# Performance work log

Measured on AMD Instinct MI355X. Metric: run time of the kernel, lower is better.

## Reference

```python
import jax, jax.numpy as jnp
import numpy as np
from jax import lax

EPS = 1e-5

def conv2d(x, w):
    # x: [B,C,H,W], w: [O,I,kh,kw], VALID, stride 1
    return lax.conv_general_dilated(x, w, (1, 1), 'VALID',
                                    dimension_numbers=('NCHW', 'OIHW', 'NCHW'))

def bn_eval(x, g, b, m, v):
    # per-channel eval-mode batchnorm on NCHW
    scale = g / jnp.sqrt(v + EPS)
    return x * scale[None, :, None, None] + (b - m * scale)[None, :, None, None]

def xcorr_depthwise(search, kernel):
    # search: [B,C,Hs,Ws], kernel: [B,C,hk,wk] -> [B,C,Ho,Wo]
    B, C, Hs, Ws = search.shape
    hk, wk = kernel.shape[2], kernel.shape[3]
    s = search.reshape(1, B * C, Hs, Ws)
    k = kernel.reshape(B * C, 1, hk, wk)
    out = lax.conv_general_dilated(s, k, (1, 1), 'VALID',
                                   dimension_numbers=('NCHW', 'OIHW', 'NCHW'),
                                   feature_group_count=B * C)
    return out.reshape(B, C, out.shape[2], out.shape[3])

def setup_inputs() -> dict:
    key = jax.random.key(0)
    ks = jax.random.split(key, 16)
    B, C, HID, OUT = 64, 256, 256, 10
    d = {}
    d['kernel'] = jax.random.normal(ks[0], (B, C, 7, 7), jnp.float32)
    d['search'] = jax.random.normal(ks[1], (B, C, 31, 31), jnp.float32)
    # conv_kernel branch
    d['ck_w'] = jax.random.normal(ks[2], (HID, C, 3, 3), jnp.float32) * 0.02
    d['ck_g'] = jnp.ones((HID,), jnp.float32)
    d['ck_b'] = jnp.zeros((HID,), jnp.float32)
    d['ck_m'] = jax.random.normal(ks[3], (HID,), jnp.float32) * 0.1
    d['ck_v'] = jax.random.uniform(ks[4], (HID,), jnp.float32, 0.5, 1.5)
    # conv_search branch
    d['cs_w'] = jax.random.normal(ks[5], (HID, C, 3, 3), jnp.float32) * 0.02
    d['cs_g'] = jnp.ones((HID,), jnp.float32)
    d['cs_b'] = jnp.zeros((HID,), jnp.float32)
    d['cs_m'] = jax.random.normal(ks[6], (HID,), jnp.float32) * 0.1
    d['cs_v'] = jax.random.uniform(ks[7], (HID,), jnp.float32, 0.5, 1.5)
    # head: 1x1 conv (no bias) + BN + ReLU + 1x1 conv (bias)
    d['h1_w'] = jax.random.normal(ks[8], (HID, HID), jnp.float32) * 0.05
    d['h_g'] = jnp.ones((HID,), jnp.float32)
    d['h_b'] = jnp.zeros((HID,), jnp.float32)
    d['h_m'] = jax.random.normal(ks[9], (HID,), jnp.float32) * 0.1
    d['h_v'] = jax.random.uniform(ks[10], (HID,), jnp.float32, 0.5, 1.5)
    d['h2_w'] = jax.random.normal(ks[11], (OUT, HID), jnp.float32) * 0.05
    d['h2_b'] = jnp.zeros((OUT,), jnp.float32)
    return d

def reference(kernel, search, ck_w, ck_g, ck_b, ck_m, ck_v,
              cs_w, cs_g, cs_b, cs_m, cs_v,
              h1_w, h_g, h_b, h_m, h_v, h2_w, h2_b):
    k = jax.nn.relu(bn_eval(conv2d(kernel, ck_w), ck_g, ck_b, ck_m, ck_v))   # [B,256,5,5]
    s = jax.nn.relu(bn_eval(conv2d(search, cs_w), cs_g, cs_b, cs_m, cs_v))   # [B,256,29,29]
    feat = xcorr_depthwise(s, k)                                             # [B,256,25,25]
    x = jnp.einsum('oi,bihw->bohw', h1_w, feat)
    x = jax.nn.relu(bn_eval(x, h_g, h_b, h_m, h_v))
    out = jnp.einsum('oi,bihw->bohw', h2_w, x) + h2_b[None, :, None, None]   # [B,10,25,25]
    return out
```

## Files before the change

kernel.cpp:

```cpp
#include <hip/hip_runtime.h>
#include <cstddef>
#include <cstdint>

#define BN_EPS 1e-5f

typedef __attribute__((ext_vector_type(8))) __bf16 bf16x8;
typedef __attribute__((ext_vector_type(4))) float f32x4;

__device__ inline unsigned short f2bf(float f) {
    unsigned u = __builtin_bit_cast(unsigned, f);
    unsigned r = (u + 0x7fff + ((u >> 16) & 1)) >> 16;
    return (unsigned short)r;
}
__device__ inline float bf2f(unsigned short u) {
    return __builtin_bit_cast(float, (unsigned)u << 16);
}

#define GLDS16(g, l)                                                        \
    __builtin_amdgcn_global_load_lds(                                       \
        (const __attribute__((address_space(1))) void*)(g),                 \
        (__attribute__((address_space(3))) void*)(l), 16, 0, 0)

template<int H, int W, int WP>
__device__ inline void nhwc_body(int bh, const float* __restrict__ in,
                                 unsigned short* __restrict__ out)
{
    __shared__ unsigned short tl[256][WP];
    const int tid = threadIdx.x;
    const int b = bh / H, h = bh - b * H;
    const int g = tid >> 5, wl = tid & 31;
    const float* base = in + (size_t)b * 256 * (H * W) + (size_t)h * W;
    if (wl < W) {
        #pragma unroll
        for (int cc = 0; cc < 32; ++cc) {
            const int c = cc * 8 + g;
            tl[c][wl] = f2bf(base[(size_t)c * (H * W) + wl]);
        }
    }
    __syncthreads();
    unsigned short* dst = out + (size_t)bh * W * 256 + tid;
    #pragma unroll
    for (int w = 0; w < W; ++w) dst[w * 256] = tl[tid][w];
}

__global__ __launch_bounds__(256)
void prep_kernel(const float* __restrict__ srch, const float* __restrict__ kin,
                 const float* __restrict__ cs_w, const float* __restrict__ ck_w,
                 const float* __restrict__ h1_w, const float* __restrict__ h2_w,
                 unsigned short* __restrict__ s16, unsigned short* __restrict__ k16,
                 unsigned short* __restrict__ wTs, unsigned short* __restrict__ wTk,
                 unsigned short* __restrict__ h1w16, unsigned short* __restrict__ h2w16,
                 int G31, int G7)
{
    const int bid = blockIdx.x;
    if (bid < G31) {
        nhwc_body<31, 31, 33>(bid, srch, s16);
    } else if (bid < G31 + G7) {
        nhwc_body<7, 7, 9>(bid - G31, kin, k16);
    } else {
        const int i = (bid - G31 - G7) * 256 + threadIdx.x;
        if (i < 589824) {
            const int ic = i & 255, t = i >> 8, oc = t & 255, khkw = t >> 8;
            wTs[i] = f2bf(cs_w[(size_t)((oc << 8) + ic) * 9 + khkw]);
        } else if (i < 1179648) {
            const int j = i - 589824;
            const int ic = j & 255, t = j >> 8, oc = t & 255, khkw = t >> 8;
            wTk[j] = f2bf(ck_w[(size_t)((oc << 8) + ic) * 9 + khkw]);
        } else if (i < 1245184) {
            const int j = i - 1179648;
            h1w16[j] = f2bf(h1_w[j]);
        } else if (i < 1249280) {
            const int j = i - 1245184;
            const int oc = j >> 8, ic = j & 255;
            h2w16[j] = (oc < 10) ? f2bf(h2_w[oc * 256 + ic]) : (unsigned short)0;
        }
    }
}

struct ConvParams {
    const unsigned short* bsrc;
    const unsigned short* wT;
    const float *bg, *bb, *bm, *bv;
    unsigned short* out;
    int IH, IW, OW, PPB, N;
};

__global__ __launch_bounds__(256)
void conv3x3_kernel(ConvParams S, ConvParams K, int Gs)
{
    __shared__ __align__(16) unsigned short Alds[128 * 64];
    __shared__ __align__(16) unsigned short Blds[128 * 64];

    const int tid  = threadIdx.x;
    const int lane = tid & 63;
    const int wid  = tid >> 6;

    const int raw = blockIdx.x;
    ConvParams P;
    int tileid;
    if (raw < Gs) {
        P = S;
        const int q8 = Gs >> 3, r8 = Gs & 7;
        const int xcd = raw & 7, seq = raw >> 3;
        tileid = (xcd < r8 ? xcd * (q8 + 1) : r8 * (q8 + 1) + (xcd - r8) * q8) + seq;
    } else {
        P = K;
        tileid = raw - Gs;
    }
    const int pt  = tileid >> 1;
    const int oct = tileid & 1;
    const int oc0 = oct << 7;
    const int p0  = pt << 7;

    int aoff[4], brow[4], bgs8[4], ldsrow[4];
    #pragma unroll
    for (int i = 0; i < 4; ++i) {
        const int r  = i * 32 + wid * 8 + (lane >> 3);
        const int gs = (lane & 7) ^ (r & 7);
        aoff[i] = (oc0 + r) * 256 + gs * 8;
        int pg = p0 + r; if (pg > P.N - 1) pg = P.N - 1;
        const int bb_ = pg / P.PPB;
        const int p   = pg - bb_ * P.PPB;
        const int oh  = p / P.OW, ow = p - oh * P.OW;
        brow[i] = (bb_ * P.IH + oh) * P.IW + ow;
        bgs8[i] = gs * 8;
        ldsrow[i] = (i * 32 + wid * 8) * 64;
    }

    const int q_  = lane >> 4;
    const int lr  = lane & 15;
    const int wm0 = (wid >> 1) * 64;
    const int wn0 = (wid & 1) * 64;
    const int g0  = q_ ^ (lane & 7);
    const int g1  = (4 + q_) ^ (lane & 7);
    const unsigned short* Abase = &Alds[(wm0 + lr) * 64];
    const unsigned short* Bbase = &Blds[(wn0 + lr) * 64];

    f32x4 acc[4][4] = {};

    int kh = 0, kw = 0;
    for (int khkw = 0; khkw < 9; ++khkw) {
        const size_t wslice = (size_t)khkw << 16;
        const int tapadd = kh * P.IW + kw;
        for (int ics = 0; ics < 4; ++ics) {
            const int ic0 = ics * 64;
            __syncthreads();
            #pragma unroll
            for (int i = 0; i < 4; ++i) {
                GLDS16(P.wT + wslice + aoff[i] + ic0, &Alds[ldsrow[i]]);
                GLDS16(P.bsrc + (size_t)(brow[i] + tapadd) * 256 + ic0 + bgs8[i],
                       &Blds[ldsrow[i]]);
            }
            __syncthreads();

            bf16x8 bfr[4][2];
            #pragma unroll
            for (int n = 0; n < 4; ++n) {
                bfr[n][0] = *(const bf16x8*)(Bbase + n * 1024 + g0 * 8);
                bfr[n][1] = *(const bf16x8*)(Bbase + n * 1024 + g1 * 8);
            }
            #pragma unroll
            for (int m = 0; m < 4; ++m) {
                bf16x8 a0 = *(const bf16x8*)(Abase + m * 1024 + g0 * 8);
                bf16x8 a1 = *(const bf16x8*)(Abase + m * 1024 + g1 * 8);
                #pragma unroll
                for (int n = 0; n < 4; ++n) {
                    acc[m][n] = __builtin_amdgcn_mfma_f32_16x16x32_bf16(
                                    a0, bfr[n][0], acc[m][n], 0, 0, 0);
                    acc[m][n] = __builtin_amdgcn_mfma_f32_16x16x32_bf16(
                                    a1, bfr[n][1], acc[m][n], 0, 0, 0);
                }
            }
        }
        if (++kw == 3) { kw = 0; ++kh; }
    }

    #pragma unroll
    for (int m = 0; m < 4; ++m) {
        const int ocm = oc0 + wm0 + m * 16 + q_ * 4;
        float sc[4], sh[4];
        #pragma unroll
        for (int r = 0; r < 4; ++r) {
            sc[r] = P.bg[ocm + r] * rsqrtf(P.bv[ocm + r] + BN_EPS);
            sh[r] = P.bb[ocm + r] - P.bm[ocm + r] * sc[r];
        }
        #pragma unroll
        for (int n = 0; n < 4; ++n) {
            const int pg = p0 + wn0 + n * 16 + lr;
            if (pg < P.N) {
                unsigned e0 = f2bf(fmaxf(acc[m][n][0] * sc[0] + sh[0], 0.f));
                unsigned e1 = f2bf(fmaxf(acc[m][n][1] * sc[1] + sh[1], 0.f));
                unsigned e2 = f2bf(fmaxf(acc[m][n][2] * sc[2] + sh[2], 0.f));
                unsigned e3 = f2bf(fmaxf(acc[m][n][3] * sc[3] + sh[3], 0.f));
                uint2 v; v.x = e0 | (e1 << 16); v.y = e2 | (e3 << 16);
                *(uint2*)(P.out + (size_t)pg * 256 + ocm) = v;
            }
        }
    }
}

__global__ __launch_bounds__(256)
void xcorr_nhwc_kernel(const unsigned short* __restrict__ sfeat,
                       const unsigned short* __restrict__ kfeat,
                       unsigned short* __restrict__ xc2)
{
    const int bid = blockIdx.x;
    const int b = bid / 25, oh = bid - b * 25;
    const int c = threadIdx.x;

    float kv[25];
    const unsigned short* kp = kfeat + (size_t)b * 25 * 256 + c;
    #pragma unroll
    for (int t = 0; t < 25; ++t) kv[t] = bf2f(kp[t * 256]);

    float acc[25];
    #pragma unroll
    for (int ow = 0; ow < 25; ++ow) acc[ow] = 0.f;

    const unsigned short* sp = sfeat + ((size_t)(b * 29 + oh)) * 29 * 256 + c;
    #pragma unroll
    for (int i = 0; i < 5; ++i) {
        #pragma unroll
        for (int w = 0; w < 29; ++w) {
            const float sv = bf2f(sp[(i * 29 + w) * 256]);
            #pragma unroll
            for (int j = 0; j < 5; ++j) {
                if (j <= w && w - j <= 24)
                    acc[w - j] += sv * kv[i * 5 + j];
            }
        }
    }

    unsigned short* op = xc2 + ((size_t)(b * 625 + oh * 25)) * 256 + c;
    #pragma unroll
    for (int ow = 0; ow < 25; ++ow) op[ow * 256] = f2bf(acc[ow]);
}

template<int KH, int KW, int IH, int IW, int OW, int PPB, bool OUT_NT>
__global__ __launch_bounds__(256)
void conv_mfma_kernel(const unsigned short* __restrict__ bsrc,
                      const unsigned short* __restrict__ wT,
                      const float* __restrict__ bn_g,
                      const float* __restrict__ bn_b,
                      const float* __restrict__ bn_m,
                      const float* __restrict__ bn_v,
                      float* __restrict__ out_f32,
                      unsigned short* __restrict__ out_nt,
                      int N)
{
    constexpr int KHW = KH * KW;
    __shared__ __align__(16) unsigned short Alds[128 * 64];
    __shared__ __align__(16) unsigned short Blds[128 * 64];

    const int tid  = threadIdx.x;
    const int lane = tid & 63;
    const int wid  = tid >> 6;

    const int NPT = (N + 127) >> 7;
    const int bid = blockIdx.x;
    const int pt  = bid % NPT;
    const int oct = bid / NPT;
    const int oc0 = oct * 128;
    const int p0  = pt * 128;

    int aoff[4], brow[4], bgs8[4], ldsrow[4];
    #pragma unroll
    for (int i = 0; i < 4; ++i) {
        const int r  = i * 32 + wid * 8 + (lane >> 3);
        const int gsv = (lane & 7) ^ (r & 7);
        aoff[i] = (oc0 + r) * 256 + gsv * 8;
        int pg = p0 + r; if (pg > N - 1) pg = N - 1;
        const int bb = pg / PPB;
        const int p  = pg - bb * PPB;
        const int oh = p / OW, ow = p - oh * OW;
        brow[i] = (bb * IH + oh) * IW + ow;
        bgs8[i] = gsv * 8;
        ldsrow[i] = (i * 32 + wid * 8) * 64;
    }

    const int q   = lane >> 4;
    const int lr  = lane & 15;
    const int wm0 = (wid >> 1) * 64;
    const int wn0 = (wid & 1) * 64;
    const int g0  = q ^ (lane & 7);
    const int g1  = (4 + q) ^ (lane & 7);
    const unsigned short* Abase = &Alds[(wm0 + lr) * 64];
    const unsigned short* Bbase = &Blds[(wn0 + lr) * 64];

    f32x4 acc[4][4] = {};

    for (int khkw = 0; khkw < KHW; ++khkw) {
        const int kh = khkw / KW;
        const int kw = khkw - kh * KW;
        const size_t wslice = (size_t)khkw * 65536;
        const int tapadd = kh * IW + kw;
        for (int ics = 0; ics < 4; ++ics) {
            const int ic0 = ics * 64;
            __syncthreads();
            #pragma unroll
            for (int i = 0; i < 4; ++i) {
                GLDS16(wT + wslice + aoff[i] + ic0, &Alds[ldsrow[i]]);
                GLDS16(bsrc + (size_t)(brow[i] + tapadd) * 256 + ic0 + bgs8[i],
                       &Blds[ldsrow[i]]);
            }
            __syncthreads();

            bf16x8 bfr[4][2];
            #pragma unroll
            for (int n = 0; n < 4; ++n) {
                bfr[n][0] = *(const bf16x8*)(Bbase + n * 1024 + g0 * 8);
                bfr[n][1] = *(const bf16x8*)(Bbase + n * 1024 + g1 * 8);
            }
            #pragma unroll
            for (int m = 0; m < 4; ++m) {
                bf16x8 a0 = *(const bf16x8*)(Abase + m * 1024 + g0 * 8);
                bf16x8 a1 = *(const bf16x8*)(Abase + m * 1024 + g1 * 8);
                #pragma unroll
                for (int n = 0; n < 4; ++n) {
                    acc[m][n] = __builtin_amdgcn_mfma_f32_16x16x32_bf16(
                                    a0, bfr[n][0], acc[m][n], 0, 0, 0);
                    acc[m][n] = __builtin_amdgcn_mfma_f32_16x16x32_bf16(
                                    a1, bfr[n][1], acc[m][n], 0, 0, 0);
                }
            }
        }
    }

    #pragma unroll
    for (int m = 0; m < 4; ++m) {
        const int ocm = oc0 + wm0 + m * 16 + q * 4;
        float sc[4], sh[4];
        #pragma unroll
        for (int r = 0; r < 4; ++r) {
            sc[r] = bn_g[ocm + r] * rsqrtf(bn_v[ocm + r] + BN_EPS);
            sh[r] = bn_b[ocm + r] - bn_m[ocm + r] * sc[r];
        }
        #pragma unroll
        for (int n = 0; n < 4; ++n) {
            const int pg = p0 + wn0 + n * 16 + lr;
            if (pg < N) {
                if (OUT_NT) {
                    unsigned e0 = f2bf(fmaxf(acc[m][n][0] * sc[0] + sh[0], 0.f));
                    unsigned e1 = f2bf(fmaxf(acc[m][n][1] * sc[1] + sh[1], 0.f));
                    unsigned e2 = f2bf(fmaxf(acc[m][n][2] * sc[2] + sh[2], 0.f));
                    unsigned e3 = f2bf(fmaxf(acc[m][n][3] * sc[3] + sh[3], 0.f));
                    uint2 v; v.x = e0 | (e1 << 16); v.y = e2 | (e3 << 16);
                    *(uint2*)(out_nt + (size_t)pg * 256 + ocm) = v;
                } else {
                    const int bb = pg / PPB;
                    const int p  = pg - bb * PPB;
                    #pragma unroll
                    for (int r = 0; r < 4; ++r)
                        out_f32[((size_t)(bb * 256 + ocm + r)) * PPB + p] =
                            fmaxf(acc[m][n][r] * sc[r] + sh[r], 0.f);
                }
            }
        }
    }
}

__global__ __launch_bounds__(256)
void head2_mfma_kernel(const unsigned short* __restrict__ y,
                       const unsigned short* __restrict__ h2w16,
                       const float* __restrict__ h2b,
                       float* __restrict__ out, int N)
{
    const int tid = threadIdx.x, lane = tid & 63, wid = tid >> 6;
    const int pbase = blockIdx.x * 256 + wid * 64;
    const int q = lane >> 4, lr = lane & 15;

    const unsigned short* arow = h2w16 + lr * 256 + q * 8;
    const unsigned short* yrow[4];
    #pragma unroll
    for (int n = 0; n < 4; ++n) {
        int pg = pbase + n * 16 + lr; if (pg > N - 1) pg = N - 1;
        yrow[n] = y + (size_t)pg * 256 + q * 8;
    }

    f32x4 acc[4] = {};
    #pragma unroll
    for (int ks = 0; ks < 8; ++ks) {
        bf16x8 a = *(const bf16x8*)(arow + ks * 32);
        #pragma unroll
        for (int n = 0; n < 4; ++n) {
            bf16x8 bb = *(const bf16x8*)(yrow[n] + ks * 32);
            acc[n] = __builtin_amdgcn_mfma_f32_16x16x32_bf16(a, bb, acc[n], 0, 0, 0);
        }
    }

    #pragma unroll
    for (int n = 0; n < 4; ++n) {
        const int pg = pbase + n * 16 + lr;
        if (pg < N) {
            const int b = pg / 625, p = pg - b * 625;
            #pragma unroll
            for (int r = 0; r < 4; ++r) {
                const int oc = q * 4 + r;
                if (oc < 10)
                    out[((size_t)(b * 10 + oc)) * 625 + p] = acc[n][r] + h2b[oc];
            }
        }
    }
}

extern "C" void kernel_launch(void* const* d_in, const int* in_sizes, int n_in,
                              void* d_out, int out_size, void* d_ws, size_t ws_size,
                              hipStream_t stream)
{
    const float* kin  = (const float*)d_in[0];
    const float* srch = (const float*)d_in[1];
    const float* ck_w = (const float*)d_in[2];
    const float* ck_g = (const float*)d_in[3];
    const float* ck_b = (const float*)d_in[4];
    const float* ck_m = (const float*)d_in[5];
    const float* ck_v = (const float*)d_in[6];
    const float* cs_w = (const float*)d_in[7];
    const float* cs_g = (const float*)d_in[8];
    const float* cs_b = (const float*)d_in[9];
    const float* cs_m = (const float*)d_in[10];
    const float* cs_v = (const float*)d_in[11];
    const float* h1_w = (const float*)d_in[12];
    const float* h_g  = (const float*)d_in[13];
    const float* h_b  = (const float*)d_in[14];
    const float* h_m  = (const float*)d_in[15];
    const float* h_v  = (const float*)d_in[16];
    const float* h2_w = (const float*)d_in[17];
    const float* h2_b = (const float*)d_in[18];

    const int B = in_sizes[0] / (256 * 7 * 7);

    uint8_t* w = (uint8_t*)d_ws;
    unsigned short* s16     = (unsigned short*)(w);
    unsigned short* xc2     = (unsigned short*)(w);
    unsigned short* sfeat16 = (unsigned short*)(w + 31490048);
    unsigned short* y       = (unsigned short*)(w + 31490048);
    unsigned short* kf16    = (unsigned short*)(w + 59047936);
    unsigned short* k16     = (unsigned short*)(w + 59867136);
    unsigned short* wTk     = (unsigned short*)(w + 61472768);
    unsigned short* wTs     = (unsigned short*)(w + 62652416);
    unsigned short* h1w16   = (unsigned short*)(w + 63832064);
    unsigned short* h2w16   = (unsigned short*)(w + 63963136);

    const int Ns = B * 841;
    const int Nk = B * 25;
    const int Nh = B * 625;
    const int Gs = 2 * ((Ns + 127) / 128);
    const int Gk = 2 * ((Nk + 127) / 128);
    const int G31 = B * 31, G7 = B * 7;

    dim3 blk(256, 1, 1);

    hipLaunchKernelGGL(prep_kernel, dim3(G31 + G7 + 4880), blk, 0, stream,
                       srch, kin, cs_w, ck_w, h1_w, h2_w,
                       s16, k16, wTs, wTk, h1w16, h2w16, G31, G7);

    ConvParams S{ s16, wTs, cs_g, cs_b, cs_m, cs_v, sfeat16, 31, 31, 29, 841, Ns };
    ConvParams K{ k16, wTk, ck_g, ck_b, ck_m, ck_v, kf16, 7, 7, 5, 25, Nk };
    hipLaunchKernelGGL(conv3x3_kernel, dim3(Gs + Gk), blk, 0, stream, S, K, Gs);

    hipLaunchKernelGGL(xcorr_nhwc_kernel, dim3(B * 25), blk, 0, stream,
                       sfeat16, kf16, xc2);

    hipLaunchKernelGGL((conv_mfma_kernel<1, 1, 25, 25, 25, 625, true>),
                       dim3(2 * ((Nh + 127) / 128)), blk, 0, stream,
                       xc2, h1w16, h_g, h_b, h_m, h_v, (float*)nullptr, y, Nh);

    hipLaunchKernelGGL(head2_mfma_kernel, dim3((Nh + 255) / 256), blk, 0, stream,
                       y, h2w16, h2_b, (float*)d_out, Nh);
}
```

Baseline: 176.6 us.

## Fuse head 1x1 conv, BN/ReLU and output projection into one kernel

Replaces the generic conv MFMA kernel for the first head layer and the separate head2 kernel with a single kernel. Each block computes all 256 hidden channels for 64 pixels, stages the BN+ReLU result in LDS, and immediately applies the 10-channel projection. This removes the global write and re-read of the bf16 intermediate y and one kernel launch. In exchange, the h1 weights are reloaded by every block, each block is smaller, and the grid assumes Nh is a multiple of 64 with no bounds check.

Result: faster. 166.6 us (-5.6%).

```diff
diff --git a/kernel.cpp b/kernel.cpp
--- a/kernel.cpp
+++ b/kernel.cpp
@@ -236,99 +236,96 @@
     for (int ow = 0; ow < 25; ++ow) op[ow * 256] = f2bf(acc[ow]);
 }
 
-template<int KH, int KW, int IH, int IW, int OW, int PPB, bool OUT_NT>
 __global__ __launch_bounds__(256)
-void conv_mfma_kernel(const unsigned short* __restrict__ bsrc,
-                      const unsigned short* __restrict__ wT,
-                      const float* __restrict__ bn_g,
-                      const float* __restrict__ bn_b,
-                      const float* __restrict__ bn_m,
-                      const float* __restrict__ bn_v,
-                      float* __restrict__ out_f32,
-                      unsigned short* __restrict__ out_nt,
-                      int N)
-{
-    constexpr int KHW = KH * KW;
-    __shared__ __align__(16) unsigned short Alds[128 * 64];
-    __shared__ __align__(16) unsigned short Blds[128 * 64];
+void fused_head_kernel(const unsigned short* __restrict__ xc2,
+                       const unsigned short* __restrict__ h1w16,
+                       const unsigned short* __restrict__ h2w16,
+                       const float* __restrict__ bn_g,
+                       const float* __restrict__ bn_b,
+                       const float* __restrict__ bn_m,
+                       const float* __restrict__ bn_v,
+                       const float* __restrict__ h2b,
+                       float* __restrict__ out)
+{
+    __shared__ __align__(16) unsigned short lds[20480];
+    unsigned short* Alds = lds;
+    unsigned short* Blds = lds + 16384;
+    unsigned short* Ylds = lds;
 
     const int tid  = threadIdx.x;
     const int lane = tid & 63;
     const int wid  = tid >> 6;
-
-    const int NPT = (N + 127) >> 7;
-    const int bid = blockIdx.x;
-    const int pt  = bid % NPT;
-    const int oct = bid / NPT;
-    const int oc0 = oct * 128;
-    const int p0  = pt * 128;
-
-    int aoff[4], brow[4], bgs8[4], ldsrow[4];
-    #pragma unroll
-    for (int i = 0; i < 4; ++i) {
-        const int r  = i * 32 + wid * 8 + (lane >> 3);
-        const int gsv = (lane & 7) ^ (r & 7);
-        aoff[i] = (oc0 + r) * 256 + gsv * 8;
-        int pg = p0 + r; if (pg > N - 1) pg = N - 1;
-        const int bb = pg / PPB;
-        const int p  = pg - bb * PPB;
-        const int oh = p / OW, ow = p - oh * OW;
-        brow[i] = (bb * IH + oh) * IW + ow;
-        bgs8[i] = gsv * 8;
-        ldsrow[i] = (i * 32 + wid * 8) * 64;
-    }
-
-    const int q   = lane >> 4;
-    const int lr  = lane & 15;
-    const int wm0 = (wid >> 1) * 64;
-    const int wn0 = (wid & 1) * 64;
-    const int g0  = q ^ (lane & 7);
-    const int g1  = (4 + q) ^ (lane & 7);
-    const unsigned short* Abase = &Alds[(wm0 + lr) * 64];
-    const unsigned short* Bbase = &Blds[(wn0 + lr) * 64];
-
-    f32x4 acc[4][4] = {};
-
-    for (int khkw = 0; khkw < KHW; ++khkw) {
-        const int kh = khkw / KW;
-        const int kw = khkw - kh * KW;
-        const size_t wslice = (size_t)khkw * 65536;
-        const int tapadd = kh * IW + kw;
-        for (int ics = 0; ics < 4; ++ics) {
-            const int ic0 = ics * 64;
-            __syncthreads();
+    const int p0   = blockIdx.x * 64;
+
+    const int lrow = lane >> 3;
+    const int gs   = 0;
+    (void)gs;
+
+    int aoffs[8], aldsr[8];
+    #pragma unroll
+    for (int s = 0; s < 8; ++s) {
+        const int rowb = s * 32 + wid * 8;
+        const int row  = rowb + lrow;
+        const int g    = (lane & 7) ^ (row & 7);
+        aoffs[s] = row * 256 + g * 8;
+        aldsr[s] = rowb * 64;
+    }
+    int boffs[2], bldsr[2];
+    #pragma unroll
+    for (int t = 0; t < 2; ++t) {
+        const int rowb = t * 32 + wid * 8;
+        const int row  = rowb + lrow;
+        const int g    = (lane & 7) ^ (row & 7);
+        boffs[t] = (p0 + row) * 256 + g * 8;
+        bldsr[t] = rowb * 64;
+    }
+
+    const int q_ = lane >> 4;
+    const int lr = lane & 15;
+    const int wm = wid >> 1;
+    const int wn = wid & 1;
+    const int g0 = q_ ^ (lane & 7);
+    const int g1 = (4 + q_) ^ (lane & 7);
+    const unsigned short* Abase = &Alds[(wm * 128 + lr) * 64];
+    const unsigned short* Bbase = &Blds[(wn * 32 + lr) * 64];
+
+    f32x4 acc[8][2] = {};
+
+    for (int ics = 0; ics < 4; ++ics) {
+        const int ic0 = ics * 64;
+        __syncthreads();
+        #pragma unroll
+        for (int s = 0; s < 8; ++s)
+            GLDS16(h1w16 + aoffs[s] + ic0, &Alds[aldsr[s]]);
+        #pragma unroll
+        for (int t = 0; t < 2; ++t)
+            GLDS16(xc2 + boffs[t] + ic0, &Blds[bldsr[t]]);
+        __syncthreads();
+
+        bf16x8 bfr[2][2];
+        #pragma unroll
+        for (int n = 0; n < 2; ++n) {
+            bfr[n][0] = *(const bf16x8*)(Bbase + n * 1024 + g0 * 8);
+            bfr[n][1] = *(const bf16x8*)(Bbase + n * 1024 + g1 * 8);
+        }
+        #pragma unroll
+        for (int m = 0; m < 8; ++m) {
+            bf16x8 a0 = *(const bf16x8*)(Abase + m * 1024 + g0 * 8);
+            bf16x8 a1 = *(const bf16x8*)(Abase + m * 1024 + g1 * 8);
             #pragma unroll
-            for (int i = 0; i < 4; ++i) {
-                GLDS16(wT + wslice + aoff[i] + ic0, &Alds[ldsrow[i]]);
-                GLDS16(bsrc + (size_t)(brow[i] + tapadd) * 256 + ic0 + bgs8[i],
-                       &Blds[ldsrow[i]]);
-            }
-            __syncthreads();
-
-            bf16x8 bfr[4][2];
-            #pragma unroll
-            for (int n = 0; n < 4; ++n) {
-                bfr[n][0] = *(const bf16x8*)(Bbase + n * 1024 + g0 * 8);
-                bfr[n][1] = *(const bf16x8*)(Bbase + n * 1024 + g1 * 8);
-            }
-            #pragma unroll
-            for (int m = 0; m < 4; ++m) {
-                bf16x8 a0 = *(const bf16x8*)(Abase + m * 1024 + g0 * 8);
-                bf16x8 a1 = *(const bf16x8*)(Abase + m * 1024 + g1 * 8);
-                #pragma unroll
-                for (int n = 0; n < 4; ++n) {
-                    acc[m][n] = __builtin_amdgcn_mfma_f32_16x16x32_bf16(
-                                    a0, bfr[n][0], acc[m][n], 0, 0, 0);
-                    acc[m][n] = __builtin_amdgcn_mfma_f32_16x16x32_bf16(
-                                    a1, bfr[n][1], acc[m][n], 0, 0, 0);
-                }
-            }
-        }
-    }
-
-    #pragma unroll
-    for (int m = 0; m < 4; ++m) {
-        const int ocm = oc0 + wm0 + m * 16 + q * 4;
+            for (int n = 0; n < 2; ++n) {
+                acc[m][n] = __builtin_amdgcn_mfma_f32_16x16x32_bf16(
+                                a0, bfr[n][0], acc[m][n], 0, 0, 0);
+                acc[m][n] = __builtin_amdgcn_mfma_f32_16x16x32_bf16(
+                                a1, bfr[n][1], acc[m][n], 0, 0, 0);
+            }
+        }
+    }
+
+    __syncthreads();
+    #pragma unroll
+    for (int m = 0; m < 8; ++m) {
+        const int ocm = wm * 128 + m * 16 + q_ * 4;
         float sc[4], sh[4];
         #pragma unroll
         for (int r = 0; r < 4; ++r) {
@@ -336,70 +333,37 @@
             sh[r] = bn_b[ocm + r] - bn_m[ocm + r] * sc[r];
         }
         #pragma unroll
-        for (int n = 0; n < 4; ++n) {
-            const int pg = p0 + wn0 + n * 16 + lr;
-            if (pg < N) {
-                if (OUT_NT) {
-                    unsigned e0 = f2bf(fmaxf(acc[m][n][0] * sc[0] + sh[0], 0.f));
-                    unsigned e1 = f2bf(fmaxf(acc[m][n][1] * sc[1] + sh[1], 0.f));
-                    unsigned e2 = f2bf(fmaxf(acc[m][n][2] * sc[2] + sh[2], 0.f));
-                    unsigned e3 = f2bf(fmaxf(acc[m][n][3] * sc[3] + sh[3], 0.f));
-                    uint2 v; v.x = e0 | (e1 << 16); v.y = e2 | (e3 << 16);
-                    *(uint2*)(out_nt + (size_t)pg * 256 + ocm) = v;
-                } else {
-                    const int bb = pg / PPB;
-                    const int p  = pg - bb * PPB;
-                    #pragma unroll
-                    for (int r = 0; r < 4; ++r)
-                        out_f32[((size_t)(bb * 256 + ocm + r)) * PPB + p] =
-                            fmaxf(acc[m][n][r] * sc[r] + sh[r], 0.f);
-                }
-            }
-        }
-    }
-}
-
-__global__ __launch_bounds__(256)
-void head2_mfma_kernel(const unsigned short* __restrict__ y,
-                       const unsigned short* __restrict__ h2w16,
-                       const float* __restrict__ h2b,
-                       float* __restrict__ out, int N)
-{
-    const int tid = threadIdx.x, lane = tid & 63, wid = tid >> 6;
-    const int pbase = blockIdx.x * 256 + wid * 64;
-    const int q = lane >> 4, lr = lane & 15;
-
-    const unsigned short* arow = h2w16 + lr * 256 + q * 8;
-    const unsigned short* yrow[4];
-    #pragma unroll
-    for (int n = 0; n < 4; ++n) {
-        int pg = pbase + n * 16 + lr; if (pg > N - 1) pg = N - 1;
-        yrow[n] = y + (size_t)pg * 256 + q * 8;
-    }
-
-    f32x4 acc[4] = {};
+        for (int n = 0; n < 2; ++n) {
+            const int pl = wn * 32 + n * 16 + lr;
+            unsigned e0 = f2bf(fmaxf(acc[m][n][0] * sc[0] + sh[0], 0.f));
+            unsigned e1 = f2bf(fmaxf(acc[m][n][1] * sc[1] + sh[1], 0.f));
+            unsigned e2 = f2bf(fmaxf(acc[m][n][2] * sc[2] + sh[2], 0.f));
+            unsigned e3 = f2bf(fmaxf(acc[m][n][3] * sc[3] + sh[3], 0.f));
+            uint2 v; v.x = e0 | (e1 << 16); v.y = e2 | (e3 << 16);
+            *(uint2*)(Ylds + (size_t)pl * 264 + ocm) = v;
+        }
+    }
+    __syncthreads();
+
+    const int pl = wid * 16 + lr;
+    const unsigned short* arow = h2w16 + lr * 256 + q_ * 8;
+    const unsigned short* brow = Ylds + (size_t)pl * 264 + q_ * 8;
+
+    f32x4 acc2 = {};
     #pragma unroll
     for (int ks = 0; ks < 8; ++ks) {
-        bf16x8 a = *(const bf16x8*)(arow + ks * 32);
-        #pragma unroll
-        for (int n = 0; n < 4; ++n) {
-            bf16x8 bb = *(const bf16x8*)(yrow[n] + ks * 32);
-            acc[n] = __builtin_amdgcn_mfma_f32_16x16x32_bf16(a, bb, acc[n], 0, 0, 0);
-        }
-    }
-
-    #pragma unroll
-    for (int n = 0; n < 4; ++n) {
-        const int pg = pbase + n * 16 + lr;
-        if (pg < N) {
-            const int b = pg / 625, p = pg - b * 625;
-            #pragma unroll
-            for (int r = 0; r < 4; ++r) {
-                const int oc = q * 4 + r;
-                if (oc < 10)
-                    out[((size_t)(b * 10 + oc)) * 625 + p] = acc[n][r] + h2b[oc];
-            }
-        }
+        bf16x8 a  = *(const bf16x8*)(arow + ks * 32);
+        bf16x8 bb = *(const bf16x8*)(brow + ks * 32);
+        acc2 = __builtin_amdgcn_mfma_f32_16x16x32_bf16(a, bb, acc2, 0, 0, 0);
+    }
+
+    const int pg = p0 + pl;
+    const int b = pg / 625, p = pg - b * 625;
+    #pragma unroll
+    for (int r = 0; r < 4; ++r) {
+        const int oc = q_ * 4 + r;
+        if (oc < 10)
+            out[((size_t)(b * 10 + oc)) * 625 + p] = acc2[r] + h2b[oc];
     }
 }
 
@@ -433,7 +397,6 @@
     unsigned short* s16     = (unsigned short*)(w);
     unsigned short* xc2     = (unsigned short*)(w);
     unsigned short* sfeat16 = (unsigned short*)(w + 31490048);
-    unsigned short* y       = (unsigned short*)(w + 31490048);
     unsigned short* kf16    = (unsigned short*)(w + 59047936);
     unsigned short* k16     = (unsigned short*)(w + 59867136);
     unsigned short* wTk     = (unsigned short*)(w + 61472768);
@@ -461,10 +424,7 @@
     hipLaunchKernelGGL(xcorr_nhwc_kernel, dim3(B * 25), blk, 0, stream,
                        sfeat16, kf16, xc2);
 
-    hipLaunchKernelGGL((conv_mfma_kernel<1, 1, 25, 25, 25, 625, true>),
-                       dim3(2 * ((Nh + 127) / 128)), blk, 0, stream,
-                       xc2, h1w16, h_g, h_b, h_m, h_v, (float*)nullptr, y, Nh);
-
-    hipLaunchKernelGGL(head2_mfma_kernel, dim3((Nh + 255) / 256), blk, 0, stream,
-                       y, h2w16, h2_b, (float*)d_out, Nh);
-}
+    hipLaunchKernelGGL(fused_head_kernel, dim3(Nh / 64), blk, 0, stream,
+                       xc2, h1w16, h2w16, h_g, h_b, h_m, h_v, h2_b,
+                       (float*)d_out);
+}
```
